# Performance work log

Measured on AMD Instinct MI355X. Metric: run time of the kernel, lower is better.

## Reference

```python
import jax, jax.numpy as jnp
import numpy as np

NEG_SLOPE = 0.1
N, D = 8192, 256


def setup_inputs() -> dict:
    key = jax.random.key(0)
    ks = jax.random.split(key, 7)
    head = jax.random.normal(ks[0], (N, D), dtype=jnp.float32)
    dependent = jax.random.normal(ks[1], (N, D), dtype=jnp.float32)
    alpha = jax.random.uniform(ks[2], (N, N), dtype=jnp.float32)
    # parameters (torch.rand init -> uniform [0,1))
    agg_weight_head = jax.random.uniform(ks[3], (D, D), dtype=jnp.float32)
    agg_weight_dependent = jax.random.uniform(ks[4], (D, D), dtype=jnp.float32)
    comb_weight_head = jax.random.uniform(ks[5], (D, D), dtype=jnp.float32)
    comb_weight_dependent = jax.random.uniform(ks[6], (D, D), dtype=jnp.float32)
    return {
        "head": head, "dependent": dependent, "alpha": alpha,
        "agg_weight_head": agg_weight_head,
        "agg_weight_dependent": agg_weight_dependent,
        "comb_weight_head": comb_weight_head,
        "comb_weight_dependent": comb_weight_dependent,
    }


def reference(head, dependent, alpha, agg_weight_head, agg_weight_dependent,
              comb_weight_head, comb_weight_dependent):
    # Double loop over j != i is equivalent to dense matmuls with the
    # diagonal contribution subtracted:
    #   head_agg[i]  = sum_j alpha[j,i]*head[j] + alpha[i,j]*dependent[j]  (j != i)
    #   dep_agg[i]   = sum_j alpha[i,j]*head[j] + alpha[j,i]*dependent[j]  (j != i)
    diag = jnp.diagonal(alpha)[:, None]                      # [N,1]
    hd_sum = head + dependent                                # [N,D]
    head_agg = alpha.T @ head + alpha @ dependent - diag * hd_sum
    dep_agg = alpha @ head + alpha.T @ dependent - diag * hd_sum
    head_out = jax.nn.leaky_relu(head_agg @ agg_weight_head + head @ comb_weight_head,
                                 negative_slope=NEG_SLOPE)
    dep_out = jax.nn.leaky_relu(dep_agg @ agg_weight_dependent + dependent @ comb_weight_dependent,
                                negative_slope=NEG_SLOPE)
    return (head_out, dep_out)
```

## Files before the change

kernel.cpp:

```cpp
#include <hip/hip_runtime.h>

#define NN 8192
#define DD 256
#define ND_ (NN * DD)

#define NEG_SLOPE 0.1f

typedef _Float16 half8 __attribute__((ext_vector_type(8)));
typedef _Float16 half4 __attribute__((ext_vector_type(4)));
typedef float f32x4 __attribute__((ext_vector_type(4)));
typedef float f32x16 __attribute__((ext_vector_type(16)));

__device__ __forceinline__ void ld_g2l16(const void* g, void* l) {
    __builtin_amdgcn_global_load_lds(
        (const __attribute__((address_space(1))) void*)g,
        (__attribute__((address_space(3))) void*)l, 16, 0, 0);
}

__device__ __forceinline__ unsigned pkhalf2(_Float16 a, _Float16 b) {
    unsigned short ua = __builtin_bit_cast(unsigned short, a);
    unsigned short ub = __builtin_bit_cast(unsigned short, b);
    return (unsigned)ua | ((unsigned)ub << 16);
}

__global__ __launch_bounds__(256, 2)
void prep_split_kernel(const float* __restrict__ h, const float* __restrict__ d,
                       _Float16* __restrict__ uS_hi, _Float16* __restrict__ vS_hi) {
    __shared__ float s_h[64 * 68];
    __shared__ float s_d[64 * 68];
    const int b  = blockIdx.x;
    const int kt = b >> 2;
    const int ct = b & 3;
    const int k0 = kt * 64;
    const int c0 = ct * 64;
    const int t  = threadIdx.x;

#pragma unroll
    for (int e = 0; e < 4; ++e) {
        int idx = e * 256 + t;
        int r   = idx >> 4;
        int c4  = (idx & 15) << 2;
        float4 hv = *(const float4*)&h[(size_t)(k0 + r) * DD + c0 + c4];
        float4 dv = *(const float4*)&d[(size_t)(k0 + r) * DD + c0 + c4];
        *(float4*)&s_h[r * 68 + c4] = hv;
        *(float4*)&s_d[r * 68 + c4] = dv;
    }
    __syncthreads();

#pragma unroll
    for (int e = 0; e < 2; ++e) {
        int idx = e * 256 + t;
        int c   = idx >> 3;
        int seg = idx & 7;
        half8 uh, vh;
#pragma unroll
        for (int m = 0; m < 8; ++m) {
            float hh = s_h[(seg * 8 + m) * 68 + c];
            float dd = s_d[(seg * 8 + m) * 68 + c];
            uh[m] = (_Float16)(hh + dd);
            vh[m] = (_Float16)(hh - dd);
        }
        int    cg   = c0 + c;
        int    kb   = kt * 2 + (seg >> 2);
        int    slot = (seg & 3) ^ ((cg >> 1) & 3);
        size_t go   = (size_t)kb * 8192 + (size_t)cg * 32 + slot * 8;
        *(half8*)&uS_hi[go] = uh;
        *(half8*)&vS_hi[go] = vh;
    }
}

__global__ __launch_bounds__(512, 4)
void agg_mfma_kernel(const float* __restrict__ alpha,
                     const _Float16* __restrict__ uS_hi, const _Float16* __restrict__ vS_hi,
                     _Float16* __restrict__ Pbuf,
                     _Float16* __restrict__ Qbuf) {
    __shared__ __align__(16) unsigned char smem[53248];
    _Float16* sS0  = (_Float16*)smem;
    _Float16* sD0  = (_Float16*)(smem + 5120);
    _Float16* sS1  = (_Float16*)(smem + 10240);
    _Float16* sD1  = (_Float16*)(smem + 15360);
    _Float16* sBu0 = (_Float16*)(smem + 20480);
    _Float16* sBv0 = (_Float16*)(smem + 28672);
    _Float16* sBu1 = (_Float16*)(smem + 36864);
    _Float16* sBv1 = (_Float16*)(smem + 45056);

    const int raw   = blockIdx.x;
    const int khalf = raw & 1;
    const int cb    = (raw >> 3) & 1;
    const int rb    = ((raw >> 1) & 3) | ((raw >> 4) << 2);
    const int I0    = rb * 64;
    const int C0    = cb * 128;
    const int t     = threadIdx.x;
    const int w     = t >> 6;
    const int lane  = t & 63;

    const bool isP = (w < 4);
    const int  cw  = w & 3;

    const _Float16* aP0 = isP ? sS0 : sD0;
    const _Float16* aP1 = isP ? sS1 : sD1;
    const _Float16* b0  = isP ? sBu0 : sBv0;
    const _Float16* b1  = isP ? sBu1 : sBv1;

    f32x16 acc0, acc1;
#pragma unroll
    for (int r = 0; r < 16; ++r) { acc0[r] = 0.f; acc1[r] = 0.f; }

    const int rbase = t & 15;
    const int kp    = (t >> 4) & 15;
    const int dup   = t >> 8;
    const int row0  = rbase + 32 * dup;
    const int lrow  = lane & 31;
    const int lk    = (lane >> 5) << 3;
    const int kbase = khalf * (NN / 2);
    const int c_local = cw * 32 + lrow;

#define LOAD_ALPHA(S, IT)                                                        \
    {                                                                            \
        const int kk0 = kbase + (IT) * 64 + 2 * kp;                              \
        size_t c0off = (size_t)kk0 * NN + I0;                                    \
        S##c00 = alpha[c0off + row0];                                            \
        S##c01 = alpha[c0off + NN + row0];                                       \
        S##c10 = alpha[c0off + row0 + 16];                                       \
        S##c11 = alpha[c0off + NN + row0 + 16];                                  \
        size_t c1off = c0off + (size_t)32 * NN;                                  \
        S##d00 = alpha[c1off + row0];                                            \
        S##d01 = alpha[c1off + NN + row0];                                       \
        S##d10 = alpha[c1off + row0 + 16];                                       \
        S##d11 = alpha[c1off + NN + row0 + 16];                                  \
        S##r00 = *(const float2*)&alpha[(size_t)(I0 + row0) * NN + kk0];         \
        S##r10 = *(const float2*)&alpha[(size_t)(I0 + row0 + 16) * NN + kk0];    \
        S##r01 = *(const float2*)&alpha[(size_t)(I0 + row0) * NN + kk0 + 32];    \
        S##r11 = *(const float2*)&alpha[(size_t)(I0 + row0 + 16) * NN + kk0 + 32]; \
    }

#define HALF(S, IT)                                                              \
    {                                                                            \
                \
                                                      \
        unsigned su0_0 = pkhalf2((_Float16)(S##c00 + S##r00.x), (_Float16)(S##c01 + S##r00.y)); \
        unsigned du0_0 = pkhalf2((_Float16)(S##c00 - S##r00.x), (_Float16)(S##c01 - S##r00.y)); \
        unsigned su1_0 = pkhalf2((_Float16)(S##c10 + S##r10.x), (_Float16)(S##c11 + S##r10.y)); \
        unsigned du1_0 = pkhalf2((_Float16)(S##c10 - S##r10.x), (_Float16)(S##c11 - S##r10.y)); \
        unsigned su0_1 = pkhalf2((_Float16)(S##d00 + S##r01.x), (_Float16)(S##d01 + S##r01.y)); \
        unsigned du0_1 = pkhalf2((_Float16)(S##d00 - S##r01.x), (_Float16)(S##d01 - S##r01.y)); \
        unsigned su1_1 = pkhalf2((_Float16)(S##d10 + S##r11.x), (_Float16)(S##d11 + S##r11.y)); \
        unsigned du1_1 = pkhalf2((_Float16)(S##d10 - S##r11.x), (_Float16)(S##d11 - S##r11.y)); \
               \
                 \
        __builtin_amdgcn_s_barrier();                                            \
                                   \
        ((unsigned*)sS0)[row0 * 20 + kp]        = su0_0;                         \
        ((unsigned*)sS0)[(row0 + 16) * 20 + kp] = su1_0;                         \
        ((unsigned*)sD0)[row0 * 20 + kp]        = du0_0;                         \
        ((unsigned*)sD0)[(row0 + 16) * 20 + kp] = du1_0;                         \
        ((unsigned*)sS1)[row0 * 20 + kp]        = su0_1;                         \
        ((unsigned*)sS1)[(row0 + 16) * 20 + kp] = su1_1;                         \
        ((unsigned*)sD1)[row0 * 20 + kp]        = du0_1;                         \
        ((unsigned*)sD1)[(row0 + 16) * 20 + kp] = du1_1;                         \
                                                    \
        {                                                                        \
            size_t gb0 = (size_t)(khalf * 128 + (IT) * 2) * 8192 + cb * 4096 +   \
                         (size_t)(w * 512 + lane * 8);                           \
            ld_g2l16(uS_hi + gb0, (unsigned char*)sBu0 + w * 1024);              \
            ld_g2l16(vS_hi + gb0, (unsigned char*)sBv0 + w * 1024);              \
            ld_g2l16(uS_hi + gb0 + 8192, (unsigned char*)sBu1 + w * 1024);       \
            ld_g2l16(vS_hi + gb0 + 8192, (unsigned char*)sBv1 + w * 1024);       \
        }                                                                        \
        __builtin_amdgcn_sched_barrier(0);      \
             \
        LOAD_ALPHA(S, (((IT) + 2) & 63))                                         \
        __builtin_amdgcn_sched_barrier(0);                                       \
                \
                        \
        asm volatile("s_waitcnt vmcnt(12)" ::: "memory");                        \
        asm volatile("s_waitcnt lgkmcnt(0)" ::: "memory");                       \
        __builtin_amdgcn_s_barrier();                                            \
        __builtin_amdgcn_sched_barrier(0);                                       \
                                                   \
        __builtin_amdgcn_s_setprio(1);                                           \
        _Pragma("unroll")                                                        \
        for (int s = 0; s < 2; ++s) {                                            \
            int gd = s * 2 + (lane >> 5);                                        \
            int sl = gd ^ ((c_local >> 1) & 3);                                  \
            int bi = c_local * 32 + sl * 8;                                      \
            half8 aH0 = *(const half8*)&aP0[(lrow) * 40 + s * 16 + lk];          \
            half8 aH1 = *(const half8*)&aP0[(32 + lrow) * 40 + s * 16 + lk];     \
            half8 bH  = *(const half8*)&b0[bi];                                  \
            acc0 = __builtin_amdgcn_mfma_f32_32x32x16_f16(aH0, bH, acc0, 0, 0, 0); \
            acc1 = __builtin_amdgcn_mfma_f32_32x32x16_f16(aH1, bH, acc1, 0, 0, 0); \
        }                                                                        \
        _Pragma("unroll")                                                        \
        for (int s = 0; s < 2; ++s) {                                            \
            int gd = s * 2 + (lane >> 5);                                        \
            int sl = gd ^ ((c_local >> 1) & 3);                                  \
            int bi = c_local * 32 + sl * 8;                                      \
            half8 aH0 = *(const half8*)&aP1[(lrow) * 40 + s * 16 + lk];          \
            half8 aH1 = *(const half8*)&aP1[(32 + lrow) * 40 + s * 16 + lk];     \
            half8 bH  = *(const half8*)&b1[bi];                                  \
            acc0 = __builtin_amdgcn_mfma_f32_32x32x16_f16(aH0, bH, acc0, 0, 0, 0); \
            acc1 = __builtin_amdgcn_mfma_f32_32x32x16_f16(aH1, bH, acc1, 0, 0, 0); \
        }                                                                        \
        __builtin_amdgcn_s_setprio(0);                                           \
    }

    float Ac00, Ac01, Ac10, Ac11, Ad00, Ad01, Ad10, Ad11;
    float2 Ar00, Ar10, Ar01, Ar11;
    float Bc00, Bc01, Bc10, Bc11, Bd00, Bd01, Bd10, Bd11;
    float2 Br00, Br10, Br01, Br11;

    LOAD_ALPHA(A, 0)
    LOAD_ALPHA(B, 1)

    for (int it2 = 0; it2 < 32; ++it2) {
        HALF(A, (it2 * 2))
        HALF(B, (it2 * 2 + 1))
    }
#undef HALF
#undef LOAD_ALPHA

    _Float16* dst = (isP ? Pbuf : Qbuf) + (size_t)khalf * ND_;
    const int colw = C0 + cw * 32 + (lane & 31);
#pragma unroll
    for (int reg = 0; reg < 16; ++reg) {
        int rr = (reg & 3) + ((reg >> 2) << 3) + ((lane >> 5) << 2);
        dst[(size_t)(I0 + rr) * DD + colw]      = (_Float16)acc0[reg];
        dst[(size_t)(I0 + 32 + rr) * DD + colw] = (_Float16)acc1[reg];
    }
}

__global__ __launch_bounds__(256, 2)
void stageB_kernel(const _Float16* __restrict__ Pbuf, const _Float16* __restrict__ Qbuf,
                   const float* __restrict__ head, const float* __restrict__ dep,
                   const float* __restrict__ alpha,
                   const float* __restrict__ Wah, const float* __restrict__ Wad,
                   const float* __restrict__ Wch, const float* __restrict__ Wcd,
                   float* __restrict__ out) {
    __shared__ float smem2[12544];
    __shared__ float s_dg[64];
    float* s_x  = smem2;
    float* s_y  = smem2 + 2176;
    float* s_w1 = smem2 + 4352;
    float* s_w2 = smem2 + 8448;

    int b   = blockIdx.x;
    int sel = b >> 8;
    int rem = b & 255;
    int rb  = rem >> 1;
    int cb  = rem & 1;
    int I0  = rb * 64;
    int C0  = cb * 128;

    const float* Y  = sel ? dep : head;
    const float* W1 = sel ? Wad : Wah;
    const float* W2 = sel ? Wcd : Wch;
    float* dst = out + sel * ND_;

    int t  = threadIdx.x;
    int rg = t & 15, cg = t >> 4;
    int r0 = rg * 4, c0 = cg * 8;

    if (t < 64) s_dg[t] = alpha[(size_t)(I0 + t) * NN + I0 + t];

    float acc[4][8];
#pragma unroll
    for (int i = 0; i < 4; ++i)
#pragma unroll
        for (int j = 0; j < 8; ++j) acc[i][j] = 0.0f;

    for (int it = 0; it < 8; ++it) {
        int k0 = it * 32;
        __syncthreads();
#pragma unroll
        for (int e = 0; e < 2; ++e) {
            int idx = e * 256 + t;
            int r   = idx >> 3;
            int k4  = (idx & 7) << 2;
            size_t go = (size_t)(I0 + r) * DD + k0 + k4;
            half4 p0 = *(const half4*)&Pbuf[go];
            half4 p1 = *(const half4*)&Pbuf[ND_ + go];
            half4 q0 = *(const half4*)&Qbuf[go];
            half4 q1 = *(const half4*)&Qbuf[ND_ + go];
            float4 hv = *(const float4*)&head[go];
            float4 dv = *(const float4*)&dep[go];
            float dgv = s_dg[r];
            float hj[4] = {hv.x, hv.y, hv.z, hv.w};
            float dj[4] = {dv.x, dv.y, dv.z, dv.w};
#pragma unroll
            for (int j = 0; j < 4; ++j) {
                float Pv = (float)p0[j] + (float)p1[j];
                float Qv = (float)q0[j] + (float)q1[j];
                float uu = hj[j] + dj[j];
                float x  = (sel ? 0.5f * (Pv - Qv) : 0.5f * (Pv + Qv)) - dgv * uu;
                s_x[(k4 + j) * 68 + r] = x;
                s_y[(k4 + j) * 68 + r] = sel ? dj[j] : hj[j];
            }
        }
#pragma unroll
        for (int e = 0; e < 4; ++e) {
            int idx = e * 256 + t;
            int kkk = idx >> 5;
            int c4  = (idx & 31) << 2;
            *(float4*)&s_w1[kkk * 128 + c4] =
                *(const float4*)&W1[(size_t)(k0 + kkk) * DD + C0 + c4];
            *(float4*)&s_w2[kkk * 128 + c4] =
                *(const float4*)&W2[(size_t)(k0 + kkk) * DD + C0 + c4];
        }
        __syncthreads();
#pragma unroll 8
        for (int k = 0; k < 32; ++k) {
            float4 xv = *(const float4*)&s_x[k * 68 + r0];
            float4 yv = *(const float4*)&s_y[k * 68 + r0];
            float4 wa = *(const float4*)&s_w1[k * 128 + c0];
            float4 wb = *(const float4*)&s_w1[k * 128 + c0 + 4];
            float4 wc = *(const float4*)&s_w2[k * 128 + c0];
            float4 wd = *(const float4*)&s_w2[k * 128 + c0 + 4];
            float xs[4]  = {xv.x, xv.y, xv.z, xv.w};
            float ys[4]  = {yv.x, yv.y, yv.z, yv.w};
            float w1s[8] = {wa.x, wa.y, wa.z, wa.w, wb.x, wb.y, wb.z, wb.w};
            float w2s[8] = {wc.x, wc.y, wc.z, wc.w, wd.x, wd.y, wd.z, wd.w};
#pragma unroll
            for (int i = 0; i < 4; ++i)
#pragma unroll
                for (int j = 0; j < 8; ++j)
                    acc[i][j] += xs[i] * w1s[j] + ys[i] * w2s[j];
        }
    }

#pragma unroll
    for (int i = 0; i < 4; ++i) {
#pragma unroll
        for (int jv = 0; jv < 2; ++jv) {
            float4 o;
            float v0 = acc[i][4 * jv + 0];
            float v1 = acc[i][4 * jv + 1];
            float v2 = acc[i][4 * jv + 2];
            float v3 = acc[i][4 * jv + 3];
            o.x = v0 >= 0.0f ? v0 : NEG_SLOPE * v0;
            o.y = v1 >= 0.0f ? v1 : NEG_SLOPE * v1;
            o.z = v2 >= 0.0f ? v2 : NEG_SLOPE * v2;
            o.w = v3 >= 0.0f ? v3 : NEG_SLOPE * v3;
            *(float4*)&dst[(size_t)(I0 + r0 + i) * DD + C0 + c0 + 4 * jv] = o;
        }
    }
}

extern "C" void kernel_launch(void* const* d_in, const int* in_sizes, int n_in,
                              void* d_out, int out_size, void* d_ws, size_t ws_size,
                              hipStream_t stream) {
    const float* head  = (const float*)d_in[0];
    const float* dep   = (const float*)d_in[1];
    const float* alpha = (const float*)d_in[2];
    const float* Wah   = (const float*)d_in[3];
    const float* Wad   = (const float*)d_in[4];
    const float* Wch   = (const float*)d_in[5];
    const float* Wcd   = (const float*)d_in[6];
    float* out = (float*)d_out;

    _Float16* ws    = (_Float16*)d_ws;
    _Float16* uS_hi = ws;
    _Float16* vS_hi = ws + (size_t)ND_;
    _Float16* Pbuf  = ws + (size_t)2 * ND_;
    _Float16* Qbuf  = ws + (size_t)4 * ND_;

    prep_split_kernel<<<512, 256, 0, stream>>>(head, dep, uS_hi, vS_hi);
    agg_mfma_kernel<<<512, 512, 0, stream>>>(alpha, uS_hi, vS_hi, Pbuf, Qbuf);
    stageB_kernel<<<512, 256, 0, stream>>>(Pbuf, Qbuf, head, dep, alpha,
                                           Wah, Wad, Wch, Wcd, out);
}
```

Measured before the change: 305.5 us.

## Drop split-K in aggregation kernel and double-buffer LDS tiles

```diff
diff --git a/kernel.cpp b/kernel.cpp
--- a/kernel.cpp
+++ b/kernel.cpp
@@ -69,38 +69,24 @@
     }
 }
 
-__global__ __launch_bounds__(512, 4)
+__global__ __launch_bounds__(512, 2)
 void agg_mfma_kernel(const float* __restrict__ alpha,
                      const _Float16* __restrict__ uS_hi, const _Float16* __restrict__ vS_hi,
                      _Float16* __restrict__ Pbuf,
                      _Float16* __restrict__ Qbuf) {
-    __shared__ __align__(16) unsigned char smem[53248];
-    _Float16* sS0  = (_Float16*)smem;
-    _Float16* sD0  = (_Float16*)(smem + 5120);
-    _Float16* sS1  = (_Float16*)(smem + 10240);
-    _Float16* sD1  = (_Float16*)(smem + 15360);
-    _Float16* sBu0 = (_Float16*)(smem + 20480);
-    _Float16* sBv0 = (_Float16*)(smem + 28672);
-    _Float16* sBu1 = (_Float16*)(smem + 36864);
-    _Float16* sBv1 = (_Float16*)(smem + 45056);
-
-    const int raw   = blockIdx.x;
-    const int khalf = raw & 1;
-    const int cb    = (raw >> 3) & 1;
-    const int rb    = ((raw >> 1) & 3) | ((raw >> 4) << 2);
-    const int I0    = rb * 64;
-    const int C0    = cb * 128;
-    const int t     = threadIdx.x;
-    const int w     = t >> 6;
-    const int lane  = t & 63;
+    __shared__ __align__(16) unsigned char smem[106496];
+
+    const int raw  = blockIdx.x;
+    const int cb   = (raw >> 3) & 1;
+    const int rb   = (raw & 7) | ((raw >> 4) << 3);
+    const int I0   = rb * 64;
+    const int C0   = cb * 128;
+    const int t    = threadIdx.x;
+    const int w    = t >> 6;
+    const int lane = t & 63;
 
     const bool isP = (w < 4);
     const int  cw  = w & 3;
-
-    const _Float16* aP0 = isP ? sS0 : sD0;
-    const _Float16* aP1 = isP ? sS1 : sD1;
-    const _Float16* b0  = isP ? sBu0 : sBv0;
-    const _Float16* b1  = isP ? sBu1 : sBv1;
 
     f32x16 acc0, acc1;
 #pragma unroll
@@ -112,12 +98,11 @@
     const int row0  = rbase + 32 * dup;
     const int lrow  = lane & 31;
     const int lk    = (lane >> 5) << 3;
-    const int kbase = khalf * (NN / 2);
     const int c_local = cw * 32 + lrow;
 
 #define LOAD_ALPHA(S, IT)                                                        \
     {                                                                            \
-        const int kk0 = kbase + (IT) * 64 + 2 * kp;                              \
+        const int kk0 = (IT) * 64 + 2 * kp;                                      \
         size_t c0off = (size_t)kk0 * NN + I0;                                    \
         S##c00 = alpha[c0off + row0];                                            \
         S##c01 = alpha[c0off + NN + row0];                                       \
@@ -134,74 +119,85 @@
         S##r11 = *(const float2*)&alpha[(size_t)(I0 + row0 + 16) * NN + kk0 + 32]; \
     }
 
-#define HALF(S, IT)                                                              \
+#define ITER(CUR, NXT, P, IT)                                                    \
     {                                                                            \
-                \
                                                       \
-        unsigned su0_0 = pkhalf2((_Float16)(S##c00 + S##r00.x), (_Float16)(S##c01 + S##r00.y)); \
-        unsigned du0_0 = pkhalf2((_Float16)(S##c00 - S##r00.x), (_Float16)(S##c01 - S##r00.y)); \
-        unsigned su1_0 = pkhalf2((_Float16)(S##c10 + S##r10.x), (_Float16)(S##c11 + S##r10.y)); \
-        unsigned du1_0 = pkhalf2((_Float16)(S##c10 - S##r10.x), (_Float16)(S##c11 - S##r10.y)); \
-        unsigned su0_1 = pkhalf2((_Float16)(S##d00 + S##r01.x), (_Float16)(S##d01 + S##r01.y)); \
-        unsigned du0_1 = pkhalf2((_Float16)(S##d00 - S##r01.x), (_Float16)(S##d01 - S##r01.y)); \
-        unsigned su1_1 = pkhalf2((_Float16)(S##d10 + S##r11.x), (_Float16)(S##d11 + S##r11.y)); \
-        unsigned du1_1 = pkhalf2((_Float16)(S##d10 - S##r11.x), (_Float16)(S##d11 - S##r11.y)); \
-               \
-                 \
-        __builtin_amdgcn_s_barrier();                                            \
-                                   \
-        ((unsigned*)sS0)[row0 * 20 + kp]        = su0_0;                         \
-        ((unsigned*)sS0)[(row0 + 16) * 20 + kp] = su1_0;                         \
-        ((unsigned*)sD0)[row0 * 20 + kp]        = du0_0;                         \
-        ((unsigned*)sD0)[(row0 + 16) * 20 + kp] = du1_0;                         \
-        ((unsigned*)sS1)[row0 * 20 + kp]        = su0_1;                         \
-        ((unsigned*)sS1)[(row0 + 16) * 20 + kp] = su1_1;                         \
-        ((unsigned*)sD1)[row0 * 20 + kp]        = du0_1;                         \
-        ((unsigned*)sD1)[(row0 + 16) * 20 + kp] = du1_1;                         \
-                                                    \
+        LOAD_ALPHA(NXT, (((IT) + 1) & 127))                                      \
+        __builtin_amdgcn_sched_barrier(0);                                       \
+                   \
+        unsigned su0_0 = pkhalf2((_Float16)(CUR##c00 + CUR##r00.x), (_Float16)(CUR##c01 + CUR##r00.y)); \
+        unsigned du0_0 = pkhalf2((_Float16)(CUR##c00 - CUR##r00.x), (_Float16)(CUR##c01 - CUR##r00.y)); \
+        unsigned su1_0 = pkhalf2((_Float16)(CUR##c10 + CUR##r10.x), (_Float16)(CUR##c11 + CUR##r10.y)); \
+        unsigned du1_0 = pkhalf2((_Float16)(CUR##c10 - CUR##r10.x), (_Float16)(CUR##c11 - CUR##r10.y)); \
+        unsigned su0_1 = pkhalf2((_Float16)(CUR##d00 + CUR##r01.x), (_Float16)(CUR##d01 + CUR##r01.y)); \
+        unsigned du0_1 = pkhalf2((_Float16)(CUR##d00 - CUR##r01.x), (_Float16)(CUR##d01 - CUR##r01.y)); \
+        unsigned su1_1 = pkhalf2((_Float16)(CUR##d10 + CUR##r11.x), (_Float16)(CUR##d11 + CUR##r11.y)); \
+        unsigned du1_1 = pkhalf2((_Float16)(CUR##d10 - CUR##r11.x), (_Float16)(CUR##d11 - CUR##r11.y)); \
+                      \
         {                                                                        \
-            size_t gb0 = (size_t)(khalf * 128 + (IT) * 2) * 8192 + cb * 4096 +   \
-                         (size_t)(w * 512 + lane * 8);                           \
-            ld_g2l16(uS_hi + gb0, (unsigned char*)sBu0 + w * 1024);              \
-            ld_g2l16(vS_hi + gb0, (unsigned char*)sBv0 + w * 1024);              \
-            ld_g2l16(uS_hi + gb0 + 8192, (unsigned char*)sBu1 + w * 1024);       \
-            ld_g2l16(vS_hi + gb0 + 8192, (unsigned char*)sBv1 + w * 1024);       \
+            unsigned* wS0 = (unsigned*)(smem + (P) * 20480);                     \
+            unsigned* wD0 = (unsigned*)(smem + (P) * 20480 + 5120);              \
+            unsigned* wS1 = (unsigned*)(smem + (P) * 20480 + 10240);             \
+            unsigned* wD1 = (unsigned*)(smem + (P) * 20480 + 15360);             \
+            wS0[row0 * 20 + kp]        = su0_0;                                  \
+            wS0[(row0 + 16) * 20 + kp] = su1_0;                                  \
+            wD0[row0 * 20 + kp]        = du0_0;                                  \
+            wD0[(row0 + 16) * 20 + kp] = du1_0;                                  \
+            wS1[row0 * 20 + kp]        = su0_1;                                  \
+            wS1[(row0 + 16) * 20 + kp] = su1_1;                                  \
+            wD1[row0 * 20 + kp]        = du0_1;                                  \
+            wD1[(row0 + 16) * 20 + kp] = du1_1;                                  \
         }                                                                        \
-        __builtin_amdgcn_sched_barrier(0);      \
+        __builtin_amdgcn_sched_barrier(0);                                       \
              \
-        LOAD_ALPHA(S, (((IT) + 2) & 63))                                         \
-        __builtin_amdgcn_sched_barrier(0);                                       \
-                \
-                        \
         asm volatile("s_waitcnt vmcnt(12)" ::: "memory");                        \
         asm volatile("s_waitcnt lgkmcnt(0)" ::: "memory");                       \
         __builtin_amdgcn_s_barrier();                                            \
         __builtin_amdgcn_sched_barrier(0);                                       \
-                                                   \
-        __builtin_amdgcn_s_setprio(1);                                           \
-        _Pragma("unroll")                                                        \
-        for (int s = 0; s < 2; ++s) {                                            \
-            int gd = s * 2 + (lane >> 5);                                        \
-            int sl = gd ^ ((c_local >> 1) & 3);                                  \
-            int bi = c_local * 32 + sl * 8;                                      \
-            half8 aH0 = *(const half8*)&aP0[(lrow) * 40 + s * 16 + lk];          \
-            half8 aH1 = *(const half8*)&aP0[(32 + lrow) * 40 + s * 16 + lk];     \
-            half8 bH  = *(const half8*)&b0[bi];                                  \
-            acc0 = __builtin_amdgcn_mfma_f32_32x32x16_f16(aH0, bH, acc0, 0, 0, 0); \
-            acc1 = __builtin_amdgcn_mfma_f32_32x32x16_f16(aH1, bH, acc1, 0, 0, 0); \
+                      \
+        {                                                                        \
+            size_t gb0 = (size_t)((((IT) + 1) & 127) * 2) * 8192 + cb * 4096 +   \
+                         (size_t)(w * 512 + lane * 8);                           \
+            unsigned char* bN = smem + 40960 + (1 - (P)) * 32768;                \
+            ld_g2l16(uS_hi + gb0,        bN + w * 1024);                         \
+            ld_g2l16(vS_hi + gb0,        bN + 8192 + w * 1024);                  \
+            ld_g2l16(uS_hi + gb0 + 8192, bN + 16384 + w * 1024);                 \
+            ld_g2l16(vS_hi + gb0 + 8192, bN + 24576 + w * 1024);                 \
         }                                                                        \
-        _Pragma("unroll")                                                        \
-        for (int s = 0; s < 2; ++s) {                                            \
-            int gd = s * 2 + (lane >> 5);                                        \
-            int sl = gd ^ ((c_local >> 1) & 3);                                  \
-            int bi = c_local * 32 + sl * 8;                                      \
-            half8 aH0 = *(const half8*)&aP1[(lrow) * 40 + s * 16 + lk];          \
-            half8 aH1 = *(const half8*)&aP1[(32 + lrow) * 40 + s * 16 + lk];     \
-            half8 bH  = *(const half8*)&b1[bi];                                  \
-            acc0 = __builtin_amdgcn_mfma_f32_32x32x16_f16(aH0, bH, acc0, 0, 0, 0); \
-            acc1 = __builtin_amdgcn_mfma_f32_32x32x16_f16(aH1, bH, acc1, 0, 0, 0); \
+        __builtin_amdgcn_sched_barrier(0);                                       \
+                                    \
+        {                                                                        \
+            const unsigned char* sdB = smem + (P) * 20480;                       \
+            const _Float16* a0p = (const _Float16*)(sdB + (isP ? 0 : 5120));     \
+            const _Float16* a1p = (const _Float16*)(sdB + 10240 + (isP ? 0 : 5120)); \
+            const unsigned char* bB = smem + 40960 + (P) * 32768;                \
+            const _Float16* b0p = (const _Float16*)(bB + (isP ? 0 : 8192));      \
+            const _Float16* b1p = (const _Float16*)(bB + 16384 + (isP ? 0 : 8192)); \
+            __builtin_amdgcn_s_setprio(1);                                       \
+            _Pragma("unroll")                                                    \
+            for (int s = 0; s < 2; ++s) {                                        \
+                int gd = s * 2 + (lane >> 5);                                    \
+                int sl = gd ^ ((c_local >> 1) & 3);                              \
+                int bi = c_local * 32 + sl * 8;                                  \
+                half8 aH0 = *(const half8*)&a0p[(lrow) * 40 + s * 16 + lk];      \
+                half8 aH1 = *(const half8*)&a0p[(32 + lrow) * 40 + s * 16 + lk]; \
+                half8 bH  = *(const half8*)&b0p[bi];                             \
+                acc0 = __builtin_amdgcn_mfma_f32_32x32x16_f16(aH0, bH, acc0, 0, 0, 0); \
+                acc1 = __builtin_amdgcn_mfma_f32_32x32x16_f16(aH1, bH, acc1, 0, 0, 0); \
+            }                                                                    \
+            _Pragma("unroll")                                                    \
+            for (int s = 0; s < 2; ++s) {                                        \
+                int gd = s * 2 + (lane >> 5);                                    \
+                int sl = gd ^ ((c_local >> 1) & 3);                              \
+                int bi = c_local * 32 + sl * 8;                                  \
+                half8 aH0 = *(const half8*)&a1p[(lrow) * 40 + s * 16 + lk];      \
+                half8 aH1 = *(const half8*)&a1p[(32 + lrow) * 40 + s * 16 + lk]; \
+                half8 bH  = *(const half8*)&b1p[bi];                             \
+                acc0 = __builtin_amdgcn_mfma_f32_32x32x16_f16(aH0, bH, acc0, 0, 0, 0); \
+                acc1 = __builtin_amdgcn_mfma_f32_32x32x16_f16(aH1, bH, acc1, 0, 0, 0); \
+            }                                                                    \
+            __builtin_amdgcn_s_setprio(0);                                       \
         }                                                                        \
-        __builtin_amdgcn_s_setprio(0);                                           \
     }
 
     float Ac00, Ac01, Ac10, Ac11, Ad00, Ad01, Ad10, Ad11;
@@ -210,16 +206,23 @@
     float2 Br00, Br10, Br01, Br11;
 
     LOAD_ALPHA(A, 0)
-    LOAD_ALPHA(B, 1)
-
-    for (int it2 = 0; it2 < 32; ++it2) {
-        HALF(A, (it2 * 2))
-        HALF(B, (it2 * 2 + 1))
-    }
-#undef HALF
+    {
+        size_t gb0 = (size_t)(w * 512 + lane * 8) + cb * 4096;
+        unsigned char* bN = smem + 40960;
+        ld_g2l16(uS_hi + gb0,        bN + w * 1024);
+        ld_g2l16(vS_hi + gb0,        bN + 8192 + w * 1024);
+        ld_g2l16(uS_hi + gb0 + 8192, bN + 16384 + w * 1024);
+        ld_g2l16(vS_hi + gb0 + 8192, bN + 24576 + w * 1024);
+    }
+
+    for (int it2 = 0; it2 < 64; ++it2) {
+        ITER(A, B, 0, (it2 * 2))
+        ITER(B, A, 1, (it2 * 2 + 1))
+    }
+#undef ITER
 #undef LOAD_ALPHA
 
-    _Float16* dst = (isP ? Pbuf : Qbuf) + (size_t)khalf * ND_;
+    _Float16* dst = isP ? Pbuf : Qbuf;
     const int colw = C0 + cw * 32 + (lane & 31);
 #pragma unroll
     for (int reg = 0; reg < 16; ++reg) {
@@ -278,9 +281,7 @@
             int k4  = (idx & 7) << 2;
             size_t go = (size_t)(I0 + r) * DD + k0 + k4;
             half4 p0 = *(const half4*)&Pbuf[go];
-            half4 p1 = *(const half4*)&Pbuf[ND_ + go];
             half4 q0 = *(const half4*)&Qbuf[go];
-            half4 q1 = *(const half4*)&Qbuf[ND_ + go];
             float4 hv = *(const float4*)&head[go];
             float4 dv = *(const float4*)&dep[go];
             float dgv = s_dg[r];
@@ -288,8 +289,8 @@
             float dj[4] = {dv.x, dv.y, dv.z, dv.w};
 #pragma unroll
             for (int j = 0; j < 4; ++j) {
-                float Pv = (float)p0[j] + (float)p1[j];
-                float Qv = (float)q0[j] + (float)q1[j];
+                float Pv = (float)p0[j];
+                float Qv = (float)q0[j];
                 float uu = hj[j] + dj[j];
                 float x  = (sel ? 0.5f * (Pv - Qv) : 0.5f * (Pv + Qv)) - dgv * uu;
                 s_x[(k4 + j) * 68 + r] = x;
@@ -361,10 +362,10 @@
     _Float16* uS_hi = ws;
     _Float16* vS_hi = ws + (size_t)ND_;
     _Float16* Pbuf  = ws + (size_t)2 * ND_;
-    _Float16* Qbuf  = ws + (size_t)4 * ND_;
+    _Float16* Qbuf  = ws + (size_t)3 * ND_;
 
     prep_split_kernel<<<512, 256, 0, stream>>>(head, dep, uS_hi, vS_hi);
-    agg_mfma_kernel<<<512, 512, 0, stream>>>(alpha, uS_hi, vS_hi, Pbuf, Qbuf);
+    agg_mfma_kernel<<<256, 512, 0, stream>>>(alpha, uS_hi, vS_hi, Pbuf, Qbuf);
     stageB_kernel<<<512, 256, 0, stream>>>(Pbuf, Qbuf, head, dep, alpha,
                                            Wah, Wad, Wch, Wcd, out);
 }
```

Result: no change. 303.6 us (-0.6%).

## Halve agg kernel column tile to 64 with 256-thread blocks and 1024-block grid

Applied to the files above, without the earlier changes.

```diff
diff --git a/kernel.cpp b/kernel.cpp
--- a/kernel.cpp
+++ b/kernel.cpp
@@ -69,38 +69,38 @@
     }
 }
 
-__global__ __launch_bounds__(512, 4)
+__global__ __launch_bounds__(256, 4)
 void agg_mfma_kernel(const float* __restrict__ alpha,
                      const _Float16* __restrict__ uS_hi, const _Float16* __restrict__ vS_hi,
                      _Float16* __restrict__ Pbuf,
                      _Float16* __restrict__ Qbuf) {
-    __shared__ __align__(16) unsigned char smem[53248];
-    _Float16* sS0  = (_Float16*)smem;
-    _Float16* sD0  = (_Float16*)(smem + 5120);
-    _Float16* sS1  = (_Float16*)(smem + 10240);
-    _Float16* sD1  = (_Float16*)(smem + 15360);
-    _Float16* sBu0 = (_Float16*)(smem + 20480);
-    _Float16* sBv0 = (_Float16*)(smem + 28672);
-    _Float16* sBu1 = (_Float16*)(smem + 36864);
-    _Float16* sBv1 = (_Float16*)(smem + 45056);
-
-    const int raw   = blockIdx.x;
-    const int khalf = raw & 1;
-    const int cb    = (raw >> 3) & 1;
-    const int rb    = ((raw >> 1) & 3) | ((raw >> 4) << 2);
-    const int I0    = rb * 64;
-    const int C0    = cb * 128;
-    const int t     = threadIdx.x;
-    const int w     = t >> 6;
-    const int lane  = t & 63;
-
-    const bool isP = (w < 4);
-    const int  cw  = w & 3;
+    __shared__ __align__(16) unsigned char smem[36864];
+    _Float16* sS0 = (_Float16*)smem;
+    _Float16* sD0 = (_Float16*)(smem + 5120);
+    _Float16* sS1 = (_Float16*)(smem + 10240);
+    _Float16* sD1 = (_Float16*)(smem + 15360);
+    _Float16* Bu0 = (_Float16*)(smem + 20480);
+    _Float16* Bv0 = (_Float16*)(smem + 24576);
+    _Float16* Bu1 = (_Float16*)(smem + 28672);
+    _Float16* Bv1 = (_Float16*)(smem + 32768);
+
+    const int raw  = blockIdx.x;
+    const int kh   = raw & 1;
+    const int cb   = (raw >> 3) & 3;
+    const int rb   = ((raw >> 1) & 3) | ((raw >> 5) << 2);
+    const int I0   = rb * 64;
+    const int C0   = cb * 64;
+    const int t    = threadIdx.x;
+    const int w    = t >> 6;
+    const int lane = t & 63;
+
+    const bool isP = (w < 2);
+    const int  cw  = w & 1;
 
     const _Float16* aP0 = isP ? sS0 : sD0;
     const _Float16* aP1 = isP ? sS1 : sD1;
-    const _Float16* b0  = isP ? sBu0 : sBv0;
-    const _Float16* b1  = isP ? sBu1 : sBv1;
+    const _Float16* b0  = isP ? Bu0 : Bv0;
+    const _Float16* b1  = isP ? Bu1 : Bv1;
 
     f32x16 acc0, acc1;
 #pragma unroll
@@ -108,118 +108,129 @@
 
     const int rbase = t & 15;
     const int kp    = (t >> 4) & 15;
-    const int dup   = t >> 8;
-    const int row0  = rbase + 32 * dup;
+    const int row0  = rbase;
+    const int row1  = rbase + 16;
+    const int row2  = rbase + 32;
+    const int row3  = rbase + 48;
     const int lrow  = lane & 31;
     const int lk    = (lane >> 5) << 3;
-    const int kbase = khalf * (NN / 2);
+    const int kbase = kh * (NN / 2);
     const int c_local = cw * 32 + lrow;
 
-#define LOAD_ALPHA(S, IT)                                                        \
-    {                                                                            \
-        const int kk0 = kbase + (IT) * 64 + 2 * kp;                              \
-        size_t c0off = (size_t)kk0 * NN + I0;                                    \
-        S##c00 = alpha[c0off + row0];                                            \
-        S##c01 = alpha[c0off + NN + row0];                                       \
-        S##c10 = alpha[c0off + row0 + 16];                                       \
-        S##c11 = alpha[c0off + NN + row0 + 16];                                  \
-        size_t c1off = c0off + (size_t)32 * NN;                                  \
-        S##d00 = alpha[c1off + row0];                                            \
-        S##d01 = alpha[c1off + NN + row0];                                       \
-        S##d10 = alpha[c1off + row0 + 16];                                       \
-        S##d11 = alpha[c1off + NN + row0 + 16];                                  \
-        S##r00 = *(const float2*)&alpha[(size_t)(I0 + row0) * NN + kk0];         \
-        S##r10 = *(const float2*)&alpha[(size_t)(I0 + row0 + 16) * NN + kk0];    \
-        S##r01 = *(const float2*)&alpha[(size_t)(I0 + row0) * NN + kk0 + 32];    \
-        S##r11 = *(const float2*)&alpha[(size_t)(I0 + row0 + 16) * NN + kk0 + 32]; \
-    }
-
-#define HALF(S, IT)                                                              \
-    {                                                                            \
+#define LOAD_ALPHA(S, IT)                                                          \
+    {                                                                              \
+        const int kk0 = kbase + (IT) * 64 + 2 * kp;                                \
+        size_t z0 = (size_t)kk0 * NN + I0;                                         \
+        size_t z1 = z0 + (size_t)32 * NN;                                          \
+        S##c000 = alpha[z0 + row0];      S##c010 = alpha[z0 + NN + row0];          \
+        S##c001 = alpha[z0 + row1];      S##c011 = alpha[z0 + NN + row1];          \
+        S##c002 = alpha[z0 + row2];      S##c012 = alpha[z0 + NN + row2];          \
+        S##c003 = alpha[z0 + row3];      S##c013 = alpha[z0 + NN + row3];          \
+        S##c100 = alpha[z1 + row0];      S##c110 = alpha[z1 + NN + row0];          \
+        S##c101 = alpha[z1 + row1];      S##c111 = alpha[z1 + NN + row1];          \
+        S##c102 = alpha[z1 + row2];      S##c112 = alpha[z1 + NN + row2];          \
+        S##c103 = alpha[z1 + row3];      S##c113 = alpha[z1 + NN + row3];          \
+        S##r00 = *(const float2*)&alpha[(size_t)(I0 + row0) * NN + kk0];           \
+        S##r01 = *(const float2*)&alpha[(size_t)(I0 + row1) * NN + kk0];           \
+        S##r02 = *(const float2*)&alpha[(size_t)(I0 + row2) * NN + kk0];           \
+        S##r03 = *(const float2*)&alpha[(size_t)(I0 + row3) * NN + kk0];           \
+        S##r10 = *(const float2*)&alpha[(size_t)(I0 + row0) * NN + kk0 + 32];      \
+        S##r11 = *(const float2*)&alpha[(size_t)(I0 + row1) * NN + kk0 + 32];      \
+        S##r12 = *(const float2*)&alpha[(size_t)(I0 + row2) * NN + kk0 + 32];      \
+        S##r13 = *(const float2*)&alpha[(size_t)(I0 + row3) * NN + kk0 + 32];      \
+    }
+
+#define HALF(CUR, NXT, IT)                                                         \
+    {                                                                              \
+                    \
+        unsigned s00 = pkhalf2((_Float16)(CUR##c000 + CUR##r00.x), (_Float16)(CUR##c010 + CUR##r00.y)); \
+        unsigned d00 = pkhalf2((_Float16)(CUR##c000 - CUR##r00.x), (_Float16)(CUR##c010 - CUR##r00.y)); \
+        unsigned s01 = pkhalf2((_Float16)(CUR##c001 + CUR##r01.x), (_Float16)(CUR##c011 + CUR##r01.y)); \
+        unsigned d01 = pkhalf2((_Float16)(CUR##c001 - CUR##r01.x), (_Float16)(CUR##c011 - CUR##r01.y)); \
+        unsigned s02 = pkhalf2((_Float16)(CUR##c002 + CUR##r02.x), (_Float16)(CUR##c012 + CUR##r02.y)); \
+        unsigned d02 = pkhalf2((_Float16)(CUR##c002 - CUR##r02.x), (_Float16)(CUR##c012 - CUR##r02.y)); \
+        unsigned s03 = pkhalf2((_Float16)(CUR##c003 + CUR##r03.x), (_Float16)(CUR##c013 + CUR##r03.y)); \
+        unsigned d03 = pkhalf2((_Float16)(CUR##c003 - CUR##r03.x), (_Float16)(CUR##c013 - CUR##r03.y)); \
+        unsigned s10 = pkhalf2((_Float16)(CUR##c100 + CUR##r10.x), (_Float16)(CUR##c110 + CUR##r10.y)); \
+        unsigned d10 = pkhalf2((_Float16)(CUR##c100 - CUR##r10.x), (_Float16)(CUR##c110 - CUR##r10.y)); \
+        unsigned s11 = pkhalf2((_Float16)(CUR##c101 + CUR##r11.x), (_Float16)(CUR##c111 + CUR##r11.y)); \
+        unsigned d11 = pkhalf2((_Float16)(CUR##c101 - CUR##r11.x), (_Float16)(CUR##c111 - CUR##r11.y)); \
+        unsigned s12 = pkhalf2((_Float16)(CUR##c102 + CUR##r12.x), (_Float16)(CUR##c112 + CUR##r12.y)); \
+        unsigned d12 = pkhalf2((_Float16)(CUR##c102 - CUR##r12.x), (_Float16)(CUR##c112 - CUR##r12.y)); \
+        unsigned s13 = pkhalf2((_Float16)(CUR##c103 + CUR##r13.x), (_Float16)(CUR##c113 + CUR##r13.y)); \
+        unsigned d13 = pkhalf2((_Float16)(CUR##c103 - CUR##r13.x), (_Float16)(CUR##c113 - CUR##r13.y)); \
+              \
+        __builtin_amdgcn_s_barrier();                                              \
+                                     \
+        ((unsigned*)sS0)[row0 * 20 + kp] = s00;  ((unsigned*)sD0)[row0 * 20 + kp] = d00; \
+        ((unsigned*)sS0)[row1 * 20 + kp] = s01;  ((unsigned*)sD0)[row1 * 20 + kp] = d01; \
+        ((unsigned*)sS0)[row2 * 20 + kp] = s02;  ((unsigned*)sD0)[row2 * 20 + kp] = d02; \
+        ((unsigned*)sS0)[row3 * 20 + kp] = s03;  ((unsigned*)sD0)[row3 * 20 + kp] = d03; \
+        ((unsigned*)sS1)[row0 * 20 + kp] = s10;  ((unsigned*)sD1)[row0 * 20 + kp] = d10; \
+        ((unsigned*)sS1)[row1 * 20 + kp] = s11;  ((unsigned*)sD1)[row1 * 20 + kp] = d11; \
+        ((unsigned*)sS1)[row2 * 20 + kp] = s12;  ((unsigned*)sD1)[row2 * 20 + kp] = d12; \
+        ((unsigned*)sS1)[row3 * 20 + kp] = s13;  ((unsigned*)sD1)[row3 * 20 + kp] = d13; \
                 \
-                                                      \
-        unsigned su0_0 = pkhalf2((_Float16)(S##c00 + S##r00.x), (_Float16)(S##c01 + S##r00.y)); \
-        unsigned du0_0 = pkhalf2((_Float16)(S##c00 - S##r00.x), (_Float16)(S##c01 - S##r00.y)); \
-        unsigned su1_0 = pkhalf2((_Float16)(S##c10 + S##r10.x), (_Float16)(S##c11 + S##r10.y)); \
-        unsigned du1_0 = pkhalf2((_Float16)(S##c10 - S##r10.x), (_Float16)(S##c11 - S##r10.y)); \
-        unsigned su0_1 = pkhalf2((_Float16)(S##d00 + S##r01.x), (_Float16)(S##d01 + S##r01.y)); \
-        unsigned du0_1 = pkhalf2((_Float16)(S##d00 - S##r01.x), (_Float16)(S##d01 - S##r01.y)); \
-        unsigned su1_1 = pkhalf2((_Float16)(S##d10 + S##r11.x), (_Float16)(S##d11 + S##r11.y)); \
-        unsigned du1_1 = pkhalf2((_Float16)(S##d10 - S##r11.x), (_Float16)(S##d11 - S##r11.y)); \
-               \
-                 \
-        __builtin_amdgcn_s_barrier();                                            \
-                                   \
-        ((unsigned*)sS0)[row0 * 20 + kp]        = su0_0;                         \
-        ((unsigned*)sS0)[(row0 + 16) * 20 + kp] = su1_0;                         \
-        ((unsigned*)sD0)[row0 * 20 + kp]        = du0_0;                         \
-        ((unsigned*)sD0)[(row0 + 16) * 20 + kp] = du1_0;                         \
-        ((unsigned*)sS1)[row0 * 20 + kp]        = su0_1;                         \
-        ((unsigned*)sS1)[(row0 + 16) * 20 + kp] = su1_1;                         \
-        ((unsigned*)sD1)[row0 * 20 + kp]        = du0_1;                         \
-        ((unsigned*)sD1)[(row0 + 16) * 20 + kp] = du1_1;                         \
-                                                    \
-        {                                                                        \
-            size_t gb0 = (size_t)(khalf * 128 + (IT) * 2) * 8192 + cb * 4096 +   \
-                         (size_t)(w * 512 + lane * 8);                           \
-            ld_g2l16(uS_hi + gb0, (unsigned char*)sBu0 + w * 1024);              \
-            ld_g2l16(vS_hi + gb0, (unsigned char*)sBv0 + w * 1024);              \
-            ld_g2l16(uS_hi + gb0 + 8192, (unsigned char*)sBu1 + w * 1024);       \
-            ld_g2l16(vS_hi + gb0 + 8192, (unsigned char*)sBv1 + w * 1024);       \
-        }                                                                        \
-        __builtin_amdgcn_sched_barrier(0);      \
-             \
-        LOAD_ALPHA(S, (((IT) + 2) & 63))                                         \
-        __builtin_amdgcn_sched_barrier(0);                                       \
+        {                                                                          \
+            size_t gb0 = (size_t)(kh * 128 + (IT) * 2) * 8192 + C0 * 32 +          \
+                         (size_t)(w * 512 + lane * 8);                             \
+            ld_g2l16(uS_hi + gb0,        (unsigned char*)Bu0 + w * 1024);          \
+            ld_g2l16(vS_hi + gb0,        (unsigned char*)Bv0 + w * 1024);          \
+            ld_g2l16(uS_hi + gb0 + 8192, (unsigned char*)Bu1 + w * 1024);          \
+            ld_g2l16(vS_hi + gb0 + 8192, (unsigned char*)Bv1 + w * 1024);          \
+        }                                                                          \
+        __builtin_amdgcn_sched_barrier(0);           \
+        LOAD_ALPHA(NXT, (((IT) + 1) & 63))                                         \
+        __builtin_amdgcn_sched_barrier(0);                                         \
                 \
-                        \
-        asm volatile("s_waitcnt vmcnt(12)" ::: "memory");                        \
-        asm volatile("s_waitcnt lgkmcnt(0)" ::: "memory");                       \
-        __builtin_amdgcn_s_barrier();                                            \
-        __builtin_amdgcn_sched_barrier(0);                                       \
-                                                   \
-        __builtin_amdgcn_s_setprio(1);                                           \
-        _Pragma("unroll")                                                        \
-        for (int s = 0; s < 2; ++s) {                                            \
-            int gd = s * 2 + (lane >> 5);                                        \
-            int sl = gd ^ ((c_local >> 1) & 3);                                  \
-            int bi = c_local * 32 + sl * 8;                                      \
-            half8 aH0 = *(const half8*)&aP0[(lrow) * 40 + s * 16 + lk];          \
-            half8 aH1 = *(const half8*)&aP0[(32 + lrow) * 40 + s * 16 + lk];     \
-            half8 bH  = *(const half8*)&b0[bi];                                  \
+        asm volatile("s_waitcnt vmcnt(24)" ::: "memory");                          \
+        asm volatile("s_waitcnt lgkmcnt(0)" ::: "memory");                         \
+        __builtin_amdgcn_s_barrier();                                              \
+        __builtin_amdgcn_sched_barrier(0);                                         \
+                                                     \
+        __builtin_amdgcn_s_setprio(1);                                             \
+        _Pragma("unroll")                                                          \
+        for (int s = 0; s < 2; ++s) {                                              \
+            int gd = s * 2 + (lane >> 5);                                          \
+            int sl = gd ^ ((c_local >> 1) & 3);                                    \
+            int bi = c_local * 32 + sl * 8;                                        \
+            half8 aH0 = *(const half8*)&aP0[(lrow) * 40 + s * 16 + lk];            \
+            half8 aH1 = *(const half8*)&aP0[(32 + lrow) * 40 + s * 16 + lk];       \
+            half8 bH  = *(const half8*)&b0[bi];                                    \
             acc0 = __builtin_amdgcn_mfma_f32_32x32x16_f16(aH0, bH, acc0, 0, 0, 0); \
             acc1 = __builtin_amdgcn_mfma_f32_32x32x16_f16(aH1, bH, acc1, 0, 0, 0); \
-        }                                                                        \
-        _Pragma("unroll")                                                        \
-        for (int s = 0; s < 2; ++s) {                                            \
-            int gd = s * 2 + (lane >> 5);                                        \
-            int sl = gd ^ ((c_local >> 1) & 3);                                  \
-            int bi = c_local * 32 + sl * 8;                                      \
-            half8 aH0 = *(const half8*)&aP1[(lrow) * 40 + s * 16 + lk];          \
-            half8 aH1 = *(const half8*)&aP1[(32 + lrow) * 40 + s * 16 + lk];     \
-            half8 bH  = *(const half8*)&b1[bi];                                  \
+        }                                                                          \
+        _Pragma("unroll")                                                          \
+        for (int s = 0; s < 2; ++s) {                                              \
+            int gd = s * 2 + (lane >> 5);                                          \
+            int sl = gd ^ ((c_local >> 1) & 3);                                    \
+            int bi = c_local * 32 + sl * 8;                                        \
+            half8 aH0 = *(const half8*)&aP1[(lrow) * 40 + s * 16 + lk];            \
+            half8 aH1 = *(const half8*)&aP1[(32 + lrow) * 40 + s * 16 + lk];       \
+            half8 bH  = *(const half8*)&b1[bi];                                    \
             acc0 = __builtin_amdgcn_mfma_f32_32x32x16_f16(aH0, bH, acc0, 0, 0, 0); \
             acc1 = __builtin_amdgcn_mfma_f32_32x32x16_f16(aH1, bH, acc1, 0, 0, 0); \
-        }                                                                        \
-        __builtin_amdgcn_s_setprio(0);                                           \
-    }
-
-    float Ac00, Ac01, Ac10, Ac11, Ad00, Ad01, Ad10, Ad11;
-    float2 Ar00, Ar10, Ar01, Ar11;
-    float Bc00, Bc01, Bc10, Bc11, Bd00, Bd01, Bd10, Bd11;
-    float2 Br00, Br10, Br01, Br11;
+        }                                                                          \
+        __builtin_amdgcn_s_setprio(0);                                             \
+    }
+
+    float Ac000, Ac010, Ac001, Ac011, Ac002, Ac012, Ac003, Ac013;
+    float Ac100, Ac110, Ac101, Ac111, Ac102, Ac112, Ac103, Ac113;
+    float2 Ar00, Ar01, Ar02, Ar03, Ar10, Ar11, Ar12, Ar13;
+    float Bc000, Bc010, Bc001, Bc011, Bc002, Bc012, Bc003, Bc013;
+    float Bc100, Bc110, Bc101, Bc111, Bc102, Bc112, Bc103, Bc113;
+    float2 Br00, Br01, Br02, Br03, Br10, Br11, Br12, Br13;
 
     LOAD_ALPHA(A, 0)
-    LOAD_ALPHA(B, 1)
 
     for (int it2 = 0; it2 < 32; ++it2) {
-        HALF(A, (it2 * 2))
-        HALF(B, (it2 * 2 + 1))
+        HALF(A, B, (it2 * 2))
+        HALF(B, A, (it2 * 2 + 1))
     }
 #undef HALF
 #undef LOAD_ALPHA
 
-    _Float16* dst = (isP ? Pbuf : Qbuf) + (size_t)khalf * ND_;
+    _Float16* dst = (isP ? Pbuf : Qbuf) + (size_t)kh * ND_;
     const int colw = C0 + cw * 32 + (lane & 31);
 #pragma unroll
     for (int reg = 0; reg < 16; ++reg) {
@@ -364,7 +375,7 @@
     _Float16* Qbuf  = ws + (size_t)4 * ND_;
 
     prep_split_kernel<<<512, 256, 0, stream>>>(head, dep, uS_hi, vS_hi);
-    agg_mfma_kernel<<<512, 512, 0, stream>>>(alpha, uS_hi, vS_hi, Pbuf, Qbuf);
+    agg_mfma_kernel<<<1024, 256, 0, stream>>>(alpha, uS_hi, vS_hi, Pbuf, Qbuf);
     stageB_kernel<<<512, 256, 0, stream>>>(Pbuf, Qbuf, head, dep, alpha,
                                            Wah, Wad, Wch, Wcd, out);
 }
```

Measured after the change: 422.5 us. +38.3%, slower.
